# Optimization experiments

Measured on AMD Instinct MI355X. Metric: run time of the kernel, lower is better.

The kernel has to match this reference:

```python
import jax, jax.numpy as jnp
import numpy as np

B, Cin, C, H, W = 2, 64, 128, 64, 64
D_INNER, N_STATE, DT_RANK, K = 256, 16, 8, 4


def _silu(x):
    return x * jax.nn.sigmoid(x)


def _layernorm(x, g, b, eps=1e-5):
    mu = x.mean(-1, keepdims=True)
    var = ((x - mu) ** 2).mean(-1, keepdims=True)
    return (x - mu) * jax.lax.rsqrt(var + eps) * g + b


def setup_inputs():
    key = jax.random.key(0)
    ks = jax.random.split(key, 16)
    f32 = jnp.float32
    inp = {}
    inp["x"] = jax.random.normal(ks[0], (B, Cin, H, W), f32)
    inp["convin_w"] = jax.random.normal(ks[1], (C, Cin), f32) * 0.05
    inp["convin_b"] = jnp.zeros((C,), f32)
    inp["ln_g"] = jnp.ones((C,), f32)
    inp["ln_b"] = jnp.zeros((C,), f32)
    inp["in_proj_w"] = jax.random.normal(ks[2], (2 * D_INNER, C), f32) * 0.05
    inp["conv_w"] = jax.random.normal(ks[3], (D_INNER, 1, 3, 3), f32) * 0.1
    inp["conv_b"] = jnp.zeros((D_INNER,), f32)
    inp["x_proj_w"] = jax.random.normal(ks[4], (K, DT_RANK + 2 * N_STATE, D_INNER), f32) * 0.05
    inp["dt_w"] = jax.random.normal(ks[5], (K, D_INNER, DT_RANK), f32) * 0.1
    inp["dt_b"] = jax.random.uniform(ks[6], (K, D_INNER), f32, -4.0, -1.0)
    inp["A_logs"] = jnp.log(jnp.tile(jnp.arange(1, N_STATE + 1, dtype=f32), (K, D_INNER, 1)))
    inp["Ds"] = jnp.ones((K, D_INNER), f32)
    inp["outnorm_g"] = jnp.ones((D_INNER,), f32)
    inp["outnorm_b"] = jnp.zeros((D_INNER,), f32)
    inp["out_proj_w"] = jax.random.normal(ks[7], (C, D_INNER), f32) * 0.05
    inp["ca_fc1_w"] = jax.random.normal(ks[8], (C // 16, C), f32) * 0.1
    inp["ca_fc2_w"] = jax.random.normal(ks[9], (C, C // 16), f32) * 0.1
    inp["gn_g"] = jnp.ones((C,), f32)
    inp["gn_b"] = jnp.zeros((C,), f32)
    return inp


def _selective_scan(u, delta, A, Bm, Cm, Ds):
    # u, delta: (B,K,d,L); A: (K,d,N); Bm, Cm: (B,K,N,L); Ds: (K,d)
    def step(h, inp):
        u_t, dt, B_t, C_t = inp
        dA = jnp.exp(dt[..., None] * A)                      # (B,K,d,N)
        h = h * dA + dt[..., None] * B_t[:, :, None, :] * u_t[..., None]
        y = jnp.einsum('bkdn,bkn->bkd', h, C_t)
        return h, y
    step = jax.checkpoint(step)
    seq = (jnp.moveaxis(u, -1, 0), jnp.moveaxis(delta, -1, 0),
           jnp.moveaxis(Bm, -1, 0), jnp.moveaxis(Cm, -1, 0))
    h0 = jnp.zeros(u.shape[:3] + (A.shape[-1],), u.dtype)
    _, ys = jax.lax.scan(step, h0, seq)                      # (L,B,K,d)
    y = jnp.moveaxis(ys, 0, -1)                              # (B,K,d,L)
    return y + u * Ds[None, :, :, None]


def reference(x, convin_w, convin_b, ln_g, ln_b, in_proj_w, conv_w, conv_b,
              x_proj_w, dt_w, dt_b, A_logs, Ds, outnorm_g, outnorm_b,
              out_proj_w, ca_fc1_w, ca_fc2_w, gn_g, gn_b):
    L = H * W
    # 1x1 conv in
    x1 = jnp.einsum('bchw,oc->bohw', x, convin_w) + convin_b[None, :, None, None]
    m = x1.transpose(0, 2, 3, 1)                             # (B,H,W,C)
    # VSSBlock: LN -> SS2D -> residual
    m_ln = _layernorm(m, ln_g, ln_b)
    xz = m_ln @ in_proj_w.T                                  # (B,H,W,2*d_inner)
    xm, z = jnp.split(xz, 2, axis=-1)
    xm = xm.transpose(0, 3, 1, 2)                            # (B,d,H,W)
    xm = jax.lax.conv_general_dilated(xm, conv_w, (1, 1), [(1, 1), (1, 1)],
                                      feature_group_count=D_INNER)
    xm = _silu(xm + conv_b[None, :, None, None])
    x_flat = xm.reshape(B, D_INNER, L)
    x_tr = xm.transpose(0, 1, 3, 2).reshape(B, D_INNER, L)
    xs = jnp.stack([x_flat, x_tr, jnp.flip(x_flat, -1), jnp.flip(x_tr, -1)], axis=1)
    x_dbl = jnp.einsum('bkdl,kcd->bkcl', xs, x_proj_w)
    dts, Bs, Cs = jnp.split(x_dbl, [DT_RANK, DT_RANK + N_STATE], axis=2)
    delta = jax.nn.softplus(jnp.einsum('bkrl,kdr->bkdl', dts, dt_w) + dt_b[None, :, :, None])
    A = -jnp.exp(A_logs)                                     # (K,d,N)
    out_y = _selective_scan(xs, delta, A, Bs, Cs, Ds)        # (B,4,d,L)
    y0 = out_y[:, 0]
    y1 = out_y[:, 1].reshape(B, D_INNER, W, H).transpose(0, 1, 3, 2).reshape(B, D_INNER, L)
    y2 = jnp.flip(out_y[:, 2], -1)
    y3 = jnp.flip(out_y[:, 3], -1).reshape(B, D_INNER, W, H).transpose(0, 1, 3, 2).reshape(B, D_INNER, L)
    y = (y0 + y1 + y2 + y3).transpose(0, 2, 1).reshape(B, H, W, D_INNER)
    y = _layernorm(y, outnorm_g, outnorm_b)
    y = y * _silu(z)
    m_out = m + y @ out_proj_w.T                             # (B,H,W,C)
    mamba = m_out.transpose(0, 3, 1, 2)                      # (B,C,H,W)
    # CBAM-style channel attention
    def mlp(v):
        return jax.nn.relu(v @ ca_fc1_w.T) @ ca_fc2_w.T
    avg = mamba.mean((2, 3))
    mx = mamba.max((2, 3))
    att = jax.nn.sigmoid(mlp(avg) + mlp(mx))[:, :, None, None]
    ca = mamba * att
    # GroupNorm(2 groups) + SiLU + residual
    g = ca.reshape(B, 2, -1)
    mu = g.mean(-1, keepdims=True)
    var = ((g - mu) ** 2).mean(-1, keepdims=True)
    g = ((g - mu) * jax.lax.rsqrt(var + 1e-5)).reshape(B, C, H, W)
    g = g * gn_g[None, :, None, None] + gn_b[None, :, None, None]
    return _silu(g) + x1
```

## Files before the change

kernel.cpp:

```cpp
#include <hip/hip_runtime.h>
#include <math.h>


#define DEV __device__ __forceinline__

DEV float sigm_(float x){ return 1.f/(1.f+__expf(-x)); }
DEV float silu_(float x){ return x*sigm_(x); }
DEV float sp_(float x){ return (x>15.f)? x : __logf(1.f+__expf(x)); }

DEV int pos_dir(int k, int l){
  switch(k&3){
    case 0: return l;
    case 1: return ((l&63)<<6)|(l>>6);
    case 2: return 4095-l;
    default:{ int m=4095-l; return ((m&63)<<6)|(m>>6); }
  }
}

#define MM4x4(av,bv) do{ \
  acc[0][0]=fmaf(av.x,bv.x,acc[0][0]); acc[0][1]=fmaf(av.x,bv.y,acc[0][1]); \
  acc[0][2]=fmaf(av.x,bv.z,acc[0][2]); acc[0][3]=fmaf(av.x,bv.w,acc[0][3]); \
  acc[1][0]=fmaf(av.y,bv.x,acc[1][0]); acc[1][1]=fmaf(av.y,bv.y,acc[1][1]); \
  acc[1][2]=fmaf(av.y,bv.z,acc[1][2]); acc[1][3]=fmaf(av.y,bv.w,acc[1][3]); \
  acc[2][0]=fmaf(av.z,bv.x,acc[2][0]); acc[2][1]=fmaf(av.z,bv.y,acc[2][1]); \
  acc[2][2]=fmaf(av.z,bv.z,acc[2][2]); acc[2][3]=fmaf(av.z,bv.w,acc[2][3]); \
  acc[3][0]=fmaf(av.w,bv.x,acc[3][0]); acc[3][1]=fmaf(av.w,bv.y,acc[3][1]); \
  acc[3][2]=fmaf(av.w,bv.z,acc[3][2]); acc[3][3]=fmaf(av.w,bv.w,acc[3][3]); \
}while(0)

__global__ __launch_bounds__(256) void k_x1ln(const float* __restrict__ x,
    const float* __restrict__ W, const float* __restrict__ bias,
    const float* __restrict__ g, const float* __restrict__ be,
    float* __restrict__ x1, float* __restrict__ mln){
  const int b=blockIdx.y, p0=blockIdx.x*64;
  __shared__ float sw[64*132];
  __shared__ float sx[64*68];
  __shared__ float red[2][16][68];
  __shared__ float smu[64], srs[64];
  const int tid=threadIdx.x, tx=tid&15, ty=tid>>4;
  for (int i=tid;i<8192;i+=256){ int c=i&63,o=i>>6; sw[c*132+o]=W[o*64+c]; }
  for (int i=tid;i<4096;i+=256){ int c=i>>6,p=i&63; sx[c*68+p]=x[((size_t)(b*64+c))*4096+p0+p]; }
  __syncthreads();
  float acc[8][4]={};
  for (int c=0;c<64;++c){
    float4 a0=*(const float4*)&sw[c*132+ty*8];
    float4 a1=*(const float4*)&sw[c*132+ty*8+4];
    float4 bv=*(const float4*)&sx[c*68+tx*4];
    acc[0][0]=fmaf(a0.x,bv.x,acc[0][0]); acc[0][1]=fmaf(a0.x,bv.y,acc[0][1]); acc[0][2]=fmaf(a0.x,bv.z,acc[0][2]); acc[0][3]=fmaf(a0.x,bv.w,acc[0][3]);
    acc[1][0]=fmaf(a0.y,bv.x,acc[1][0]); acc[1][1]=fmaf(a0.y,bv.y,acc[1][1]); acc[1][2]=fmaf(a0.y,bv.z,acc[1][2]); acc[1][3]=fmaf(a0.y,bv.w,acc[1][3]);
    acc[2][0]=fmaf(a0.z,bv.x,acc[2][0]); acc[2][1]=fmaf(a0.z,bv.y,acc[2][1]); acc[2][2]=fmaf(a0.z,bv.z,acc[2][2]); acc[2][3]=fmaf(a0.z,bv.w,acc[2][3]);
    acc[3][0]=fmaf(a0.w,bv.x,acc[3][0]); acc[3][1]=fmaf(a0.w,bv.y,acc[3][1]); acc[3][2]=fmaf(a0.w,bv.z,acc[3][2]); acc[3][3]=fmaf(a0.w,bv.w,acc[3][3]);
    acc[4][0]=fmaf(a1.x,bv.x,acc[4][0]); acc[4][1]=fmaf(a1.x,bv.y,acc[4][1]); acc[4][2]=fmaf(a1.x,bv.z,acc[4][2]); acc[4][3]=fmaf(a1.x,bv.w,acc[4][3]);
    acc[5][0]=fmaf(a1.y,bv.x,acc[5][0]); acc[5][1]=fmaf(a1.y,bv.y,acc[5][1]); acc[5][2]=fmaf(a1.y,bv.z,acc[5][2]); acc[5][3]=fmaf(a1.y,bv.w,acc[5][3]);
    acc[6][0]=fmaf(a1.z,bv.x,acc[6][0]); acc[6][1]=fmaf(a1.z,bv.y,acc[6][1]); acc[6][2]=fmaf(a1.z,bv.z,acc[6][2]); acc[6][3]=fmaf(a1.z,bv.w,acc[6][3]);
    acc[7][0]=fmaf(a1.w,bv.x,acc[7][0]); acc[7][1]=fmaf(a1.w,bv.y,acc[7][1]); acc[7][2]=fmaf(a1.w,bv.z,acc[7][2]); acc[7][3]=fmaf(a1.w,bv.w,acc[7][3]);
  }
  float xr[8][4];
  #pragma unroll
  for (int i=0;i<8;++i){
    float bs=bias[ty*8+i];
    #pragma unroll
    for (int j=0;j<4;++j) xr[i][j]=acc[i][j]+bs;
  }
  {
    float s[4]={},s2[4]={};
    #pragma unroll
    for (int i=0;i<8;++i)
      #pragma unroll
      for (int j=0;j<4;++j){ s[j]+=xr[i][j]; s2[j]=fmaf(xr[i][j],xr[i][j],s2[j]); }
    #pragma unroll
    for (int j=0;j<4;++j){ red[0][ty][tx*4+j]=s[j]; red[1][ty][tx*4+j]=s2[j]; }
  }
  __syncthreads();
  if (tid<64){
    float S=0.f,S2=0.f;
    #pragma unroll
    for (int t=0;t<16;++t){ S+=red[0][t][tid]; S2+=red[1][t][tid]; }
    float mu=S*(1.f/128.f), var=S2*(1.f/128.f)-mu*mu;
    smu[tid]=mu; srs[tid]=rsqrtf(var+1e-5f);
  }
  __syncthreads();
  float* lnt=sw;
  #pragma unroll
  for (int i=0;i<8;++i){
    int o=ty*8+i;
    float gv=g[o], bev=be[o];
    #pragma unroll
    for (int j=0;j<4;++j){
      int p=tx*4+j;
      lnt[o*66+p]=(xr[i][j]-smu[p])*srs[p]*gv+bev;
    }
    *(float4*)&x1[((size_t)(b*128+o))*4096+p0+tx*4]=make_float4(xr[i][0],xr[i][1],xr[i][2],xr[i][3]);
  }
  __syncthreads();
  for (int i=tid;i<8192;i+=256){ int p=i>>7,o=i&127; mln[((size_t)(b*4096+p0+p))*128+o]=lnt[o*66+p]; }
}

__global__ __launch_bounds__(256) void k_inproj(const float* __restrict__ mln,
    const float* __restrict__ W, float* __restrict__ xmpre_t, float* __restrict__ z){
  const int m0=blockIdx.y*64, n0=blockIdx.x*64;
  __shared__ float As[16][68], Bs[16][68];
  const int tid=threadIdx.x, tx=tid&15, ty=tid>>4;
  float acc[4][4]={};
  for (int k0=0;k0<128;k0+=16){
    for (int i=tid;i<64*16;i+=256){ int m=i>>4,k=i&15; As[k][m]=mln[(size_t)(m0+m)*128+(k0+k)]; }
    for (int i=tid;i<64*16;i+=256){ int n=i>>4,k=i&15; Bs[k][n]=W[(size_t)(n0+n)*128+(k0+k)]; }
    __syncthreads();
    #pragma unroll
    for (int k=0;k<16;++k){
      float4 av=*(const float4*)&As[k][ty*4];
      float4 bv=*(const float4*)&Bs[k][tx*4];
      MM4x4(av,bv);
    }
    __syncthreads();
  }
  const int col=n0+tx*4;
  #pragma unroll
  for (int i=0;i<4;++i){
    int row=m0+ty*4+i;
    float4 v=make_float4(acc[i][0],acc[i][1],acc[i][2],acc[i][3]);
    if (col<256) *(float4*)&xmpre_t[(size_t)row*256+col]=v;
    else         *(float4*)&z[(size_t)row*256+(col-256)]=v;
  }
}

__global__ __launch_bounds__(256) void k_dwconv(const float* __restrict__ xmpre_t,
    const float* __restrict__ cw, const float* __restrict__ cb, float* __restrict__ xflat_t){
  __shared__ float sw[2304];
  __shared__ float sb[256];
  const int tid=threadIdx.x;
  for (int i=tid;i<2304;i+=256) sw[i]=cw[i];
  sb[tid]=cb[tid];
  __syncthreads();
  const int bp0=blockIdx.x*16;
  const int b=bp0>>12, p0=bp0&4095;
  const int dq=tid&63, pg=tid>>6;
  const int d0=dq*4;
  float wr[9][4];
  #pragma unroll
  for (int t=0;t<9;++t)
    #pragma unroll
    for (int c=0;c<4;++c) wr[t][c]=sw[(d0+c)*9+t];
  const float4 bias=make_float4(sb[d0],sb[d0+1],sb[d0+2],sb[d0+3]);
  #pragma unroll
  for (int j=0;j<4;++j){
    const int p=p0+pg*4+j;
    const int h=p>>6, w=p&63;
    float4 acc=bias;
    #pragma unroll
    for (int dh=-1;dh<=1;++dh){
      int hh=h+dh; if ((unsigned)hh>=64u) continue;
      #pragma unroll
      for (int dw=-1;dw<=1;++dw){
        int ww=w+dw; if ((unsigned)ww>=64u) continue;
        const int t=(dh+1)*3+(dw+1);
        float4 iv=*(const float4*)&xmpre_t[((size_t)((b<<12)+hh*64+ww))*256+d0];
        acc.x=fmaf(iv.x,wr[t][0],acc.x); acc.y=fmaf(iv.y,wr[t][1],acc.y);
        acc.z=fmaf(iv.z,wr[t][2],acc.z); acc.w=fmaf(iv.w,wr[t][3],acc.w);
      }
    }
    acc.x=silu_(acc.x); acc.y=silu_(acc.y); acc.z=silu_(acc.z); acc.w=silu_(acc.w);
    *(float4*)&xflat_t[((size_t)((b<<12)+p))*256+d0]=acc;
  }
}

__global__ __launch_bounds__(256) void k_proj(const float* __restrict__ xflat_t,
    const float* __restrict__ xpw, float* __restrict__ pdt, float* __restrict__ pbc){
  const int b=blockIdx.z, n0=blockIdx.y*32, m0=blockIdx.x*64;
  __shared__ float As[16][68], Bs[16][36];
  const int tid=threadIdx.x, tx=tid&15, ty=tid>>4;
  float acc[4][2]={};
  for (int k0=0;k0<256;k0+=16){
    for (int i=tid;i<64*16;i+=256){ int m=i>>4,kk=i&15; As[kk][m]=xflat_t[((size_t)((b<<12)+m0+m))*256+k0+kk]; }
    for (int i=tid;i<32*16;i+=256){ int n=i>>4,kk=i&15; Bs[kk][n]=xpw[(size_t)(n0+n)*256+k0+kk]; }
    __syncthreads();
    #pragma unroll
    for (int kk=0;kk<16;++kk){
      float4 av=*(const float4*)&As[kk][ty*4];
      float2 bv=*(const float2*)&Bs[kk][tx*2];
      acc[0][0]=fmaf(av.x,bv.x,acc[0][0]); acc[0][1]=fmaf(av.x,bv.y,acc[0][1]);
      acc[1][0]=fmaf(av.y,bv.x,acc[1][0]); acc[1][1]=fmaf(av.y,bv.y,acc[1][1]);
      acc[2][0]=fmaf(av.z,bv.x,acc[2][0]); acc[2][1]=fmaf(av.z,bv.y,acc[2][1]);
      acc[3][0]=fmaf(av.w,bv.x,acc[3][0]); acc[3][1]=fmaf(av.w,bv.y,acc[3][1]);
    }
    __syncthreads();
  }
  #pragma unroll
  for (int i=0;i<4;++i){
    int l=m0+ty*4+i;
    #pragma unroll
    for (int j=0;j<2;++j){
      int r=n0+tx*2+j, kd=r/40, c=r%40, bk=b*4+kd;
      float v=acc[i][j];
      if (c<8) pdt[((size_t)bk*4096+l)*8+c]=v;
      else     pbc[((size_t)bk*4096+l)*32+(c-8)]=v;
    }
  }
}

__global__ __launch_bounds__(256) void k_scanA(const float* __restrict__ pdt,
    const float* __restrict__ pbc, const float* __restrict__ xflat_t,
    const float* __restrict__ dtw, const float* __restrict__ dtb,
    const float* __restrict__ A_logs, const float* __restrict__ Ds,
    float* __restrict__ Pc, float* __restrict__ He, float* __restrict__ y4){
  const int bx=blockIdx.x;
  const int ch=bx&127, k=(bx>>7)&3, b=bx>>9, bk=b*4+k;
  const int d=threadIdx.x;
  __shared__ float sbc[1024];
  __shared__ float sdt[256];
  for (int i=d;i<1024;i+=256) sbc[i]=pbc[((size_t)bk*4096+(ch<<5))*32+i];
  sdt[d]=pdt[((size_t)bk*4096+(ch<<5))*8+d];
  const float* ap=&A_logs[((k<<8)+d)<<4];
  const float ac0=-__expf(ap[0]);
  bool pw=true;
  #pragma unroll
  for (int n=1;n<16;++n){ float an_=-__expf(ap[n]); pw=pw&&(fabsf(an_-(float)(n+1)*ac0)<=1e-4f*fabsf(an_)); }
  float w8[8];
  {
    float4 w0=*(const float4*)&dtw[(size_t)k*2048+d*8];
    float4 w1=*(const float4*)&dtw[(size_t)k*2048+d*8+4];
    w8[0]=w0.x;w8[1]=w0.y;w8[2]=w0.z;w8[3]=w0.w;w8[4]=w1.x;w8[5]=w1.y;w8[6]=w1.z;w8[7]=w1.w;
  }
  const float dtbd=dtb[(k<<8)+d];
  const float dsv=Ds[(k<<8)+d];
  __syncthreads();
  float h[16]; float sdv=0.f;
  #pragma unroll
  for (int n=0;n<16;++n) h[n]=0.f;
  const float* up=xflat_t+((size_t)b<<12)*256+d;
  if (pw){
    for (int s=0;s<32;++s){
      const int l=(ch<<5)+s;
      float t=dtbd;
      #pragma unroll
      for (int r=0;r<8;++r) t=fmaf(sdt[s*8+r],w8[r],t);
      const float dv=sp_(t);
      const float u=up[(size_t)pos_dir(k,l)*256];
      const float dvu=dv*u;
      sdv+=dv;
      const float q=__expf(dv*ac0);
      float an=q, yl=0.f;
      #pragma unroll
      for (int n4=0;n4<4;++n4){
        float4 bb=*(const float4*)&sbc[s*32+n4*4];
        float4 cc=*(const float4*)&sbc[s*32+16+n4*4];
        h[n4*4+0]=fmaf(h[n4*4+0],an,dvu*bb.x); yl=fmaf(h[n4*4+0],cc.x,yl); an*=q;
        h[n4*4+1]=fmaf(h[n4*4+1],an,dvu*bb.y); yl=fmaf(h[n4*4+1],cc.y,yl); an*=q;
        h[n4*4+2]=fmaf(h[n4*4+2],an,dvu*bb.z); yl=fmaf(h[n4*4+2],cc.z,yl); an*=q;
        h[n4*4+3]=fmaf(h[n4*4+3],an,dvu*bb.w); yl=fmaf(h[n4*4+3],cc.w,yl); an*=q;
      }
      y4[((size_t)((b<<12)+pos_dir(k,l))*4+k)*256+d]=yl+u*dsv;
    }
  } else {
    float acoef[16];
    #pragma unroll
    for (int n=0;n<16;++n) acoef[n]=-__expf(ap[n]);
    for (int s=0;s<32;++s){
      const int l=(ch<<5)+s;
      float t=dtbd;
      #pragma unroll
      for (int r=0;r<8;++r) t=fmaf(sdt[s*8+r],w8[r],t);
      const float dv=sp_(t);
      const float u=up[(size_t)pos_dir(k,l)*256];
      const float dvu=dv*u;
      sdv+=dv;
      float yl=0.f;
      #pragma unroll
      for (int n=0;n<16;++n){
        float a=__expf(dv*acoef[n]);
        h[n]=fmaf(h[n],a,dvu*sbc[s*32+n]);
        yl=fmaf(h[n],sbc[s*32+16+n],yl);
      }
      y4[((size_t)((b<<12)+pos_dir(k,l))*4+k)*256+d]=yl+u*dsv;
    }
  }
  const size_t obase=(size_t)ch*32768 + ((size_t)bk*256+d)*16;
  if (pw){
    const float qe=__expf(ac0*sdv);
    float an=qe, pcv[16];
    #pragma unroll
    for (int n=0;n<16;++n){ pcv[n]=an; an*=qe; }
    #pragma unroll
    for (int n4=0;n4<4;++n4) *(float4*)&Pc[obase+n4*4]=make_float4(pcv[n4*4],pcv[n4*4+1],pcv[n4*4+2],pcv[n4*4+3]);
  } else {
    #pragma unroll
    for (int n=0;n<16;++n) Pc[obase+n]=__expf(-__expf(ap[n])*sdv);
  }
  #pragma unroll
  for (int n4=0;n4<4;++n4) *(float4*)&He[obase+n4*4]=make_float4(h[n4*4],h[n4*4+1],h[n4*4+2],h[n4*4+3]);
}

__global__ __launch_bounds__(256) void k_scanB(const float* Pc, const float* He, float* Hin){
  const int g2=threadIdx.x&63, tc=threadIdx.x>>6;
  const int gid=blockIdx.x*64+g2;
  float p[32], e[32];
  #pragma unroll
  for (int i=0;i<32;++i){
    size_t idx=(size_t)(tc*32+i)*32768+gid;
    p[i]=Pc[idx]; e[i]=He[idx];
  }
  float P=1.f, E=0.f;
  #pragma unroll
  for (int i=0;i<32;++i){ E=fmaf(E,p[i],e[i]); P*=p[i]; }
  __shared__ float sP[4][64], sE[4][64];
  sP[tc][g2]=P; sE[tc][g2]=E;
  __syncthreads();
  float Hp=0.f;
  for (int t=0;t<tc;++t) Hp=fmaf(Hp,sP[t][g2],sE[t][g2]);
  #pragma unroll
  for (int i=0;i<32;++i){
    Hin[(size_t)(tc*32+i)*32768+gid]=Hp;
    Hp=fmaf(Hp,p[i],e[i]);
  }
}

__global__ __launch_bounds__(256) void k_scanC2(const float* __restrict__ pdt,
    const float* __restrict__ pbc, const float* __restrict__ dtw,
    const float* __restrict__ dtb, const float* __restrict__ A_logs,
    const float* __restrict__ Hin, float* __restrict__ y4){
  const int bx=blockIdx.x;
  const int ch=bx&127, k=(bx>>7)&3, b=bx>>9, bk=b*4+k;
  if (ch==0) return;
  const int d=threadIdx.x;
  __shared__ float sC[512];
  __shared__ float sdt[256];
  for (int i=d;i<512;i+=256){ int s=i>>4,n=i&15; sC[i]=pbc[((size_t)bk*4096+(ch<<5)+s)*32+16+n]; }
  sdt[d]=pdt[((size_t)bk*4096+(ch<<5))*8+d];
  const float* ap=&A_logs[((k<<8)+d)<<4];
  const float ac0=-__expf(ap[0]);
  bool pw=true;
  #pragma unroll
  for (int n=1;n<16;++n){ float an_=-__expf(ap[n]); pw=pw&&(fabsf(an_-(float)(n+1)*ac0)<=1e-4f*fabsf(an_)); }
  float w8[8];
  {
    float4 w0=*(const float4*)&dtw[(size_t)k*2048+d*8];
    float4 w1=*(const float4*)&dtw[(size_t)k*2048+d*8+4];
    w8[0]=w0.x;w8[1]=w0.y;w8[2]=w0.z;w8[3]=w0.w;w8[4]=w1.x;w8[5]=w1.y;w8[6]=w1.z;w8[7]=w1.w;
  }
  const float dtbd=dtb[(k<<8)+d];
  __syncthreads();
  const size_t ibase=(size_t)ch*32768 + ((size_t)bk*256+d)*16;
  float h[16];
  #pragma unroll
  for (int n4=0;n4<4;++n4){
    float4 hv=*(const float4*)&Hin[ibase+n4*4];
    h[n4*4]=hv.x; h[n4*4+1]=hv.y; h[n4*4+2]=hv.z; h[n4*4+3]=hv.w;
  }
  if (pw){
    float cumd=0.f;
    for (int s=0;s<32;++s){
      float t=dtbd;
      #pragma unroll
      for (int r=0;r<8;++r) t=fmaf(sdt[s*8+r],w8[r],t);
      cumd+=sp_(t);
      const float q=__expf(ac0*cumd);
      float an=q, corr=0.f;
      #pragma unroll
      for (int n4=0;n4<4;++n4){
        float4 cc=*(const float4*)&sC[s*16+n4*4];
        corr=fmaf(h[n4*4+0]*an,cc.x,corr); an*=q;
        corr=fmaf(h[n4*4+1]*an,cc.y,corr); an*=q;
        corr=fmaf(h[n4*4+2]*an,cc.z,corr); an*=q;
        corr=fmaf(h[n4*4+3]*an,cc.w,corr); an*=q;
      }
      const int l=(ch<<5)+s;
      y4[((size_t)((b<<12)+pos_dir(k,l))*4+k)*256+d]+=corr;
    }
  } else {
    float acoef[16];
    #pragma unroll
    for (int n=0;n<16;++n) acoef[n]=-__expf(ap[n]);
    float cumd=0.f;
    for (int s=0;s<32;++s){
      float t=dtbd;
      #pragma unroll
      for (int r=0;r<8;++r) t=fmaf(sdt[s*8+r],w8[r],t);
      cumd+=sp_(t);
      float corr=0.f;
      #pragma unroll
      for (int n=0;n<16;++n) corr=fmaf(h[n]*__expf(acoef[n]*cumd),sC[s*16+n],corr);
      const int l=(ch<<5)+s;
      y4[((size_t)((b<<12)+pos_dir(k,l))*4+k)*256+d]+=corr;
    }
  }
}

__global__ __launch_bounds__(256) void k_outnorm(const float* __restrict__ y4,
    const float* __restrict__ g, const float* __restrict__ be,
    const float* __restrict__ z, float* __restrict__ yg){
  const int bp=blockIdx.x, d=threadIdx.x;
  const float* base=y4+(size_t)bp*1024;
  float v=base[d]+base[256+d]+base[512+d]+base[768+d];
  float s=v, s2=v*v;
  #pragma unroll
  for (int m=1;m<64;m<<=1){ s+=__shfl_xor(s,m); s2+=__shfl_xor(s2,m); }
  __shared__ float rs[4], rs2[4];
  if ((d&63)==0){ rs[d>>6]=s; rs2[d>>6]=s2; }
  __syncthreads();
  float S=rs[0]+rs[1]+rs[2]+rs[3], S2=rs2[0]+rs2[1]+rs2[2]+rs2[3];
  float mu=S*(1.f/256.f), var=S2*(1.f/256.f)-mu*mu, rstd=rsqrtf(var+1e-5f);
  float ln=(v-mu)*rstd*g[d]+be[d];
  float zv=z[(size_t)bp*256+d];
  yg[(size_t)bp*256+d]=ln*silu_(zv);
}

__global__ __launch_bounds__(256) void k_outproj(const float* __restrict__ yg,
    const float* __restrict__ W, const float* __restrict__ x1, float* __restrict__ mamba){
  const int b=blockIdx.z, m0=blockIdx.y*64, n0=blockIdx.x*64;
  __shared__ float As[16][68], Bs[16][68];
  const int tid=threadIdx.x, tx=tid&15, ty=tid>>4;
  float acc[4][4]={};
  const float* Yb=yg+(size_t)(b<<12)*256;
  for (int k0=0;k0<256;k0+=16){
    for (int i=tid;i<64*16;i+=256){ int m=i>>4,k=i&15; As[k][m]=W[(size_t)(m0+m)*256+(k0+k)]; }
    for (int i=tid;i<64*16;i+=256){ int n=i>>4,k=i&15; Bs[k][n]=Yb[(size_t)(n0+n)*256+(k0+k)]; }
    __syncthreads();
    #pragma unroll
    for (int k=0;k<16;++k){
      float4 av=*(const float4*)&As[k][ty*4];
      float4 bv=*(const float4*)&Bs[k][tx*4];
      MM4x4(av,bv);
    }
    __syncthreads();
  }
  #pragma unroll
  for (int i=0;i<4;++i){
    int c=m0+ty*4+i;
    size_t base=(size_t)((b<<7)+c)*4096 + n0+tx*4;
    float4 xv=*(const float4*)&x1[base];
    float4 v=make_float4(acc[i][0]+xv.x,acc[i][1]+xv.y,acc[i][2]+xv.z,acc[i][3]+xv.w);
    *(float4*)&mamba[base]=v;
  }
}

__global__ __launch_bounds__(256) void k_stats(const float* __restrict__ mamba, float* __restrict__ stats){
  const int bc=blockIdx.x, tid=threadIdx.x;
  const float* row=mamba+(size_t)bc*4096;
  float s=0.f,s2=0.f,mx=-3.402823466e38f;
  for (int i=tid;i<4096;i+=256){ float v=row[i]; s+=v; s2=fmaf(v,v,s2); mx=fmaxf(mx,v); }
  #pragma unroll
  for (int m=1;m<64;m<<=1){
    s+=__shfl_xor(s,m); s2+=__shfl_xor(s2,m); mx=fmaxf(mx,__shfl_xor(mx,m));
  }
  __shared__ float r0[4],r1[4],r2[4];
  if ((tid&63)==0){ int wv=tid>>6; r0[wv]=s; r1[wv]=s2; r2[wv]=mx; }
  __syncthreads();
  if (tid==0){
    stats[bc*3+0]=r0[0]+r0[1]+r0[2]+r0[3];
    stats[bc*3+1]=r1[0]+r1[1]+r1[2]+r1[3];
    stats[bc*3+2]=fmaxf(fmaxf(r2[0],r2[1]),fmaxf(r2[2],r2[3]));
  }
}

__global__ __launch_bounds__(256) void k_att(const float* __restrict__ stats,
    const float* __restrict__ fc1, const float* __restrict__ fc2,
    float* __restrict__ att, float* __restrict__ gstat){
  __shared__ float avg[2][128], mxs[2][128], S1[2][128], S2[2][128], hsum[2][8], attv[2][128];
  const int tid=threadIdx.x, b=tid>>7, c=tid&127;
  float s1=stats[tid*3], s2=stats[tid*3+1], m=stats[tid*3+2];
  avg[b][c]=s1*(1.f/4096.f); mxs[b][c]=m; S1[b][c]=s1; S2[b][c]=s2;
  __syncthreads();
  if (tid<16){
    int bb=tid>>3, i=tid&7;
    float ha=0.f,hm=0.f;
    for (int cc=0;cc<128;++cc){ float w=fc1[i*128+cc]; ha=fmaf(w,avg[bb][cc],ha); hm=fmaf(w,mxs[bb][cc],hm); }
    hsum[bb][i]=fmaxf(ha,0.f)+fmaxf(hm,0.f);
  }
  __syncthreads();
  float sacc=0.f;
  #pragma unroll
  for (int i=0;i<8;++i) sacc=fmaf(fc2[c*8+i],hsum[b][i],sacc);
  float a=sigm_(sacc);
  attv[b][c]=a; att[tid]=a;
  __syncthreads();
  if (tid<4){
    int bb=tid>>1, gp=tid&1;
    float sum1=0.f,sum2=0.f;
    for (int cc=0;cc<64;++cc){
      int c2=gp*64+cc; float av=attv[bb][c2];
      sum1=fmaf(av,S1[bb][c2],sum1);
      sum2=fmaf(av*av,S2[bb][c2],sum2);
    }
    const float inv=1.f/(64.f*4096.f);
    float mu=sum1*inv, ex2=sum2*inv, var=ex2-mu*mu;
    gstat[tid*2]=mu; gstat[tid*2+1]=rsqrtf(var+1e-5f);
  }
}

__global__ __launch_bounds__(256) void k_final(const float* __restrict__ mamba,
    const float* __restrict__ x1, const float* __restrict__ att,
    const float* __restrict__ gstat, const float* __restrict__ gg,
    const float* __restrict__ gb, float* __restrict__ out){
  const int idx=blockIdx.x*256+threadIdx.x;
  const int c=(idx>>12)&127, b=idx>>19;
  const int grp=(b<<1)+(c>>6);
  float v=mamba[idx]*att[(b<<7)+c];
  float vn=(v-gstat[grp*2])*gstat[grp*2+1]*gg[c]+gb[c];
  out[idx]=silu_(vn)+x1[idx];
}

extern "C" void kernel_launch(void* const* d_in, const int* in_sizes, int n_in,
                              void* d_out, int out_size, void* d_ws, size_t ws_size,
                              hipStream_t stream){
  (void)in_sizes; (void)n_in; (void)out_size; (void)ws_size;
  const float* x        =(const float*)d_in[0];
  const float* convin_w =(const float*)d_in[1];
  const float* convin_b =(const float*)d_in[2];
  const float* ln_g     =(const float*)d_in[3];
  const float* ln_b     =(const float*)d_in[4];
  const float* in_proj_w=(const float*)d_in[5];
  const float* conv_w   =(const float*)d_in[6];
  const float* conv_b   =(const float*)d_in[7];
  const float* x_proj_w =(const float*)d_in[8];
  const float* dt_w     =(const float*)d_in[9];
  const float* dt_b     =(const float*)d_in[10];
  const float* A_logs   =(const float*)d_in[11];
  const float* Ds       =(const float*)d_in[12];
  const float* outnorm_g=(const float*)d_in[13];
  const float* outnorm_b=(const float*)d_in[14];
  const float* out_proj_w=(const float*)d_in[15];
  const float* ca_fc1_w =(const float*)d_in[16];
  const float* ca_fc2_w =(const float*)d_in[17];
  const float* gn_g     =(const float*)d_in[18];
  const float* gn_b     =(const float*)d_in[19];

  float* ws=(float*)d_ws;
  float* x1     =ws+0;
  float* z      =ws+1048576;
  float* xmpre_t=ws+3145728;
  float* mln    =ws+5242880;
  float* xflat_t=ws+6291456;
  float* pdt    =ws+8388608;
  float* pbc    =ws+8912896;
  float* Pc     =ws+10485760;
  float* He     =ws+14680064;
  float* y4     =ws+18874368;
  float* yg     =ws+3145728;
  float* mamba  =ws+5242880;
  float* stats  =ws+27262976;
  float* att    =stats+768;
  float* gstat  =att+256;

  const dim3 blk(256);
  k_x1ln   <<<dim3(64,2),   blk,0,stream>>>(x, convin_w, convin_b, ln_g, ln_b, x1, mln);
  k_inproj <<<dim3(8,128),  blk,0,stream>>>(mln, in_proj_w, xmpre_t, z);
  k_dwconv <<<dim3(512),    blk,0,stream>>>(xmpre_t, conv_w, conv_b, xflat_t);
  k_proj   <<<dim3(64,5,2), blk,0,stream>>>(xflat_t, x_proj_w, pdt, pbc);
  k_scanA  <<<dim3(1024),   blk,0,stream>>>(pdt, pbc, xflat_t, dt_w, dt_b, A_logs, Ds, Pc, He, y4);
  k_scanB  <<<dim3(512),    blk,0,stream>>>(Pc, He, Pc );
  k_scanC2 <<<dim3(1024),   blk,0,stream>>>(pdt, pbc, dt_w, dt_b, A_logs, Pc , y4);
  k_outnorm<<<dim3(8192),   blk,0,stream>>>(y4, outnorm_g, outnorm_b, z, yg);
  k_outproj<<<dim3(64,2,2), blk,0,stream>>>(yg, out_proj_w, x1, mamba);
  k_stats  <<<dim3(256),    blk,0,stream>>>(mamba, stats);
  k_att    <<<dim3(1),      blk,0,stream>>>(stats, ca_fc1_w, ca_fc2_w, att, gstat);
  k_final  <<<dim3(4096),   blk,0,stream>>>(mamba, x1, att, gstat, gn_g, gn_b, (float*)d_out);
}
```

Before: 301.7 us.

## Use bf16 MFMA for projections and atomically accumulate scan outputs

Replaces the three FP32 shared-memory SIMT GEMMs (in_proj, x_proj, out_proj) with bf16 MFMA 16x16x32 kernels that load fragments straight from global memory. The intermediate activations (LN output, conv output, gated output) are stored as bf16, halving their traffic. The scan kernels now atomically add into a single summed y buffer instead of writing four per-direction copies, which drops the 4-way read in outnorm at the cost of atomic contention and an extra memset. The changes trade accuracy (bf16 operands), and per-lane scalar epilogue stores are less coalesced.

```diff
diff --git a/kernel.cpp b/kernel.cpp
--- a/kernel.cpp
+++ b/kernel.cpp
@@ -3,10 +3,20 @@
 
 
 #define DEV __device__ __forceinline__
+
+typedef __attribute__((ext_vector_type(8))) short bf16x8;
+typedef __attribute__((ext_vector_type(4))) float f32x4;
 
 DEV float sigm_(float x){ return 1.f/(1.f+__expf(-x)); }
 DEV float silu_(float x){ return x*sigm_(x); }
 DEV float sp_(float x){ return (x>15.f)? x : __logf(1.f+__expf(x)); }
+
+DEV unsigned short f2bf(float f){
+  union{float f; unsigned u;} v; v.f=f;
+  unsigned r=v.u + 0x7FFFu + ((v.u>>16)&1u);
+  return (unsigned short)(r>>16);
+}
+DEV float bf2f(unsigned short h){ union{unsigned u; float f;} v; v.u=((unsigned)h)<<16; return v.f; }
 
 DEV int pos_dir(int k, int l){
   switch(k&3){
@@ -17,21 +27,18 @@
   }
 }
 
-#define MM4x4(av,bv) do{ \
-  acc[0][0]=fmaf(av.x,bv.x,acc[0][0]); acc[0][1]=fmaf(av.x,bv.y,acc[0][1]); \
-  acc[0][2]=fmaf(av.x,bv.z,acc[0][2]); acc[0][3]=fmaf(av.x,bv.w,acc[0][3]); \
-  acc[1][0]=fmaf(av.y,bv.x,acc[1][0]); acc[1][1]=fmaf(av.y,bv.y,acc[1][1]); \
-  acc[1][2]=fmaf(av.y,bv.z,acc[1][2]); acc[1][3]=fmaf(av.y,bv.w,acc[1][3]); \
-  acc[2][0]=fmaf(av.z,bv.x,acc[2][0]); acc[2][1]=fmaf(av.z,bv.y,acc[2][1]); \
-  acc[2][2]=fmaf(av.z,bv.z,acc[2][2]); acc[2][3]=fmaf(av.z,bv.w,acc[2][3]); \
-  acc[3][0]=fmaf(av.w,bv.x,acc[3][0]); acc[3][1]=fmaf(av.w,bv.y,acc[3][1]); \
-  acc[3][2]=fmaf(av.w,bv.z,acc[3][2]); acc[3][3]=fmaf(av.w,bv.w,acc[3][3]); \
-}while(0)
+DEV bf16x8 cvt_frag(const float* p){
+  float4 q0=*(const float4*)p, q1=*(const float4*)(p+4);
+  bf16x8 t;
+  t[0]=(short)f2bf(q0.x); t[1]=(short)f2bf(q0.y); t[2]=(short)f2bf(q0.z); t[3]=(short)f2bf(q0.w);
+  t[4]=(short)f2bf(q1.x); t[5]=(short)f2bf(q1.y); t[6]=(short)f2bf(q1.z); t[7]=(short)f2bf(q1.w);
+  return t;
+}
 
 __global__ __launch_bounds__(256) void k_x1ln(const float* __restrict__ x,
     const float* __restrict__ W, const float* __restrict__ bias,
     const float* __restrict__ g, const float* __restrict__ be,
-    float* __restrict__ x1, float* __restrict__ mln){
+    float* __restrict__ x1, unsigned short* __restrict__ mlnb){
   const int b=blockIdx.y, p0=blockIdx.x*64;
   __shared__ float sw[64*132];
   __shared__ float sx[64*68];
@@ -93,39 +100,50 @@
     *(float4*)&x1[((size_t)(b*128+o))*4096+p0+tx*4]=make_float4(xr[i][0],xr[i][1],xr[i][2],xr[i][3]);
   }
   __syncthreads();
-  for (int i=tid;i<8192;i+=256){ int p=i>>7,o=i&127; mln[((size_t)(b*4096+p0+p))*128+o]=lnt[o*66+p]; }
-}
-
-__global__ __launch_bounds__(256) void k_inproj(const float* __restrict__ mln,
+  for (int i=tid;i<8192;i+=256){ int p=i>>7,o=i&127; mlnb[((size_t)(b*4096+p0+p))*128+o]=f2bf(lnt[o*66+p]); }
+}
+
+__global__ __launch_bounds__(256) void k_inproj(const unsigned short* __restrict__ mlnb,
     const float* __restrict__ W, float* __restrict__ xmpre_t, float* __restrict__ z){
-  const int m0=blockIdx.y*64, n0=blockIdx.x*64;
-  __shared__ float As[16][68], Bs[16][68];
-  const int tid=threadIdx.x, tx=tid&15, ty=tid>>4;
-  float acc[4][4]={};
-  for (int k0=0;k0<128;k0+=16){
-    for (int i=tid;i<64*16;i+=256){ int m=i>>4,k=i&15; As[k][m]=mln[(size_t)(m0+m)*128+(k0+k)]; }
-    for (int i=tid;i<64*16;i+=256){ int n=i>>4,k=i&15; Bs[k][n]=W[(size_t)(n0+n)*128+(k0+k)]; }
-    __syncthreads();
-    #pragma unroll
-    for (int k=0;k<16;++k){
-      float4 av=*(const float4*)&As[k][ty*4];
-      float4 bv=*(const float4*)&Bs[k][tx*4];
-      MM4x4(av,bv);
-    }
-    __syncthreads();
-  }
-  const int col=n0+tx*4;
-  #pragma unroll
-  for (int i=0;i<4;++i){
-    int row=m0+ty*4+i;
-    float4 v=make_float4(acc[i][0],acc[i][1],acc[i][2],acc[i][3]);
-    if (col<256) *(float4*)&xmpre_t[(size_t)row*256+col]=v;
-    else         *(float4*)&z[(size_t)row*256+(col-256)]=v;
-  }
+  const int wave=threadIdx.x>>6, lane=threadIdx.x&63;
+  const int quad=lane>>4, l16=lane&15;
+  const int m0=blockIdx.y*128+(wave>>1)*64;
+  const int n0=blockIdx.x*64+(wave&1)*32;
+  f32x4 acc[4][2];
+  #pragma unroll
+  for (int i=0;i<4;++i)
+    #pragma unroll
+    for (int j=0;j<2;++j) acc[i][j]=(f32x4){0.f,0.f,0.f,0.f};
+  for (int k0=0;k0<128;k0+=32){
+    bf16x8 a[4], b[2];
+    #pragma unroll
+    for (int mi=0;mi<4;++mi)
+      a[mi]=*(const bf16x8*)&mlnb[(size_t)(m0+mi*16+l16)*128 + k0 + quad*8];
+    #pragma unroll
+    for (int ni=0;ni<2;++ni)
+      b[ni]=cvt_frag(&W[(size_t)(n0+ni*16+l16)*128 + k0 + quad*8]);
+    #pragma unroll
+    for (int mi=0;mi<4;++mi)
+      #pragma unroll
+      for (int ni=0;ni<2;++ni)
+        acc[mi][ni]=__builtin_amdgcn_mfma_f32_16x16x32_bf16(a[mi],b[ni],acc[mi][ni],0,0,0);
+  }
+  #pragma unroll
+  for (int mi=0;mi<4;++mi)
+    #pragma unroll
+    for (int ni=0;ni<2;++ni)
+      #pragma unroll
+      for (int r=0;r<4;++r){
+        const int row=m0+mi*16+quad*4+r;
+        const int col=n0+ni*16+l16;
+        float v=acc[mi][ni][r];
+        if (col<256) xmpre_t[(size_t)row*256+col]=v;
+        else         z[(size_t)row*256+(col-256)]=v;
+      }
 }
 
 __global__ __launch_bounds__(256) void k_dwconv(const float* __restrict__ xmpre_t,
-    const float* __restrict__ cw, const float* __restrict__ cb, float* __restrict__ xflat_t){
+    const float* __restrict__ cw, const float* __restrict__ cb, unsigned short* __restrict__ xflatb){
   __shared__ float sw[2304];
   __shared__ float sb[256];
   const int tid=threadIdx.x;
@@ -159,50 +177,58 @@
         acc.z=fmaf(iv.z,wr[t][2],acc.z); acc.w=fmaf(iv.w,wr[t][3],acc.w);
       }
     }
-    acc.x=silu_(acc.x); acc.y=silu_(acc.y); acc.z=silu_(acc.z); acc.w=silu_(acc.w);
-    *(float4*)&xflat_t[((size_t)((b<<12)+p))*256+d0]=acc;
-  }
-}
-
-__global__ __launch_bounds__(256) void k_proj(const float* __restrict__ xflat_t,
+    ushort4 o;
+    o.x=f2bf(silu_(acc.x)); o.y=f2bf(silu_(acc.y)); o.z=f2bf(silu_(acc.z)); o.w=f2bf(silu_(acc.w));
+    *(ushort4*)&xflatb[((size_t)((b<<12)+p))*256+d0]=o;
+  }
+}
+
+__global__ __launch_bounds__(256) void k_proj(const unsigned short* __restrict__ xflatb,
     const float* __restrict__ xpw, float* __restrict__ pdt, float* __restrict__ pbc){
-  const int b=blockIdx.z, n0=blockIdx.y*32, m0=blockIdx.x*64;
-  __shared__ float As[16][68], Bs[16][36];
-  const int tid=threadIdx.x, tx=tid&15, ty=tid>>4;
-  float acc[4][2]={};
-  for (int k0=0;k0<256;k0+=16){
-    for (int i=tid;i<64*16;i+=256){ int m=i>>4,kk=i&15; As[kk][m]=xflat_t[((size_t)((b<<12)+m0+m))*256+k0+kk]; }
-    for (int i=tid;i<32*16;i+=256){ int n=i>>4,kk=i&15; Bs[kk][n]=xpw[(size_t)(n0+n)*256+k0+kk]; }
-    __syncthreads();
-    #pragma unroll
-    for (int kk=0;kk<16;++kk){
-      float4 av=*(const float4*)&As[kk][ty*4];
-      float2 bv=*(const float2*)&Bs[kk][tx*2];
-      acc[0][0]=fmaf(av.x,bv.x,acc[0][0]); acc[0][1]=fmaf(av.x,bv.y,acc[0][1]);
-      acc[1][0]=fmaf(av.y,bv.x,acc[1][0]); acc[1][1]=fmaf(av.y,bv.y,acc[1][1]);
-      acc[2][0]=fmaf(av.z,bv.x,acc[2][0]); acc[2][1]=fmaf(av.z,bv.y,acc[2][1]);
-      acc[3][0]=fmaf(av.w,bv.x,acc[3][0]); acc[3][1]=fmaf(av.w,bv.y,acc[3][1]);
-    }
-    __syncthreads();
-  }
-  #pragma unroll
-  for (int i=0;i<4;++i){
-    int l=m0+ty*4+i;
-    #pragma unroll
-    for (int j=0;j<2;++j){
-      int r=n0+tx*2+j, kd=r/40, c=r%40, bk=b*4+kd;
-      float v=acc[i][j];
-      if (c<8) pdt[((size_t)bk*4096+l)*8+c]=v;
-      else     pbc[((size_t)bk*4096+l)*32+(c-8)]=v;
-    }
-  }
+  const int wave=threadIdx.x>>6, lane=threadIdx.x&63;
+  const int quad=lane>>4, l16=lane&15;
+  const int m0=(wave&1)*80;
+  const int n0=blockIdx.x*64+(wave>>1)*32;
+  f32x4 acc[5][2];
+  #pragma unroll
+  for (int i=0;i<5;++i)
+    #pragma unroll
+    for (int j=0;j<2;++j) acc[i][j]=(f32x4){0.f,0.f,0.f,0.f};
+  for (int k0=0;k0<256;k0+=32){
+    bf16x8 a[5], b[2];
+    #pragma unroll
+    for (int mi=0;mi<5;++mi)
+      a[mi]=cvt_frag(&xpw[(size_t)(m0+mi*16+l16)*256 + k0 + quad*8]);
+    #pragma unroll
+    for (int ni=0;ni<2;++ni)
+      b[ni]=*(const bf16x8*)&xflatb[(size_t)(n0+ni*16+l16)*256 + k0 + quad*8];
+    #pragma unroll
+    for (int mi=0;mi<5;++mi)
+      #pragma unroll
+      for (int ni=0;ni<2;++ni)
+        acc[mi][ni]=__builtin_amdgcn_mfma_f32_16x16x32_bf16(a[mi],b[ni],acc[mi][ni],0,0,0);
+  }
+  #pragma unroll
+  for (int mi=0;mi<5;++mi)
+    #pragma unroll
+    for (int ni=0;ni<2;++ni)
+      #pragma unroll
+      for (int r=0;r<4;++r){
+        const int rr=m0+mi*16+quad*4+r;
+        const int col=n0+ni*16+l16;
+        const int b_=col>>12, pos=col&4095;
+        const int kd=rr/40, c=rr%40, bk=b_*4+kd;
+        float v=acc[mi][ni][r];
+        if (c<8) pdt[((size_t)bk*4096+pos)*8+c]=v;
+        else     pbc[((size_t)bk*4096+pos)*32+(c-8)]=v;
+      }
 }
 
 __global__ __launch_bounds__(256) void k_scanA(const float* __restrict__ pdt,
-    const float* __restrict__ pbc, const float* __restrict__ xflat_t,
+    const float* __restrict__ pbc, const unsigned short* __restrict__ xflatb,
     const float* __restrict__ dtw, const float* __restrict__ dtb,
     const float* __restrict__ A_logs, const float* __restrict__ Ds,
-    float* __restrict__ Pc, float* __restrict__ He, float* __restrict__ y4){
+    float* __restrict__ Pc, float* __restrict__ He, float* __restrict__ ysum){
   const int bx=blockIdx.x;
   const int ch=bx&127, k=(bx>>7)&3, b=bx>>9, bk=b*4+k;
   const int d=threadIdx.x;
@@ -227,7 +253,7 @@
   float h[16]; float sdv=0.f;
   #pragma unroll
   for (int n=0;n<16;++n) h[n]=0.f;
-  const float* up=xflat_t+((size_t)b<<12)*256+d;
+  const unsigned short* up=xflatb+((size_t)b<<12)*256+d;
   if (pw){
     for (int s=0;s<32;++s){
       const int l=(ch<<5)+s;
@@ -235,7 +261,8 @@
       #pragma unroll
       for (int r=0;r<8;++r) t=fmaf(sdt[s*8+r],w8[r],t);
       const float dv=sp_(t);
-      const float u=up[(size_t)pos_dir(k,l)*256];
+      const int pos=pos_dir(k,l);
+      const float u=bf2f(up[(size_t)pos*256]);
       const float dvu=dv*u;
       sdv+=dv;
       const float q=__expf(dv*ac0);
@@ -249,7 +276,7 @@
         h[n4*4+2]=fmaf(h[n4*4+2],an,dvu*bb.z); yl=fmaf(h[n4*4+2],cc.z,yl); an*=q;
         h[n4*4+3]=fmaf(h[n4*4+3],an,dvu*bb.w); yl=fmaf(h[n4*4+3],cc.w,yl); an*=q;
       }
-      y4[((size_t)((b<<12)+pos_dir(k,l))*4+k)*256+d]=yl+u*dsv;
+      atomicAdd(&ysum[((size_t)((b<<12)+pos))*256+d], yl+u*dsv);
     }
   } else {
     float acoef[16];
@@ -261,7 +288,8 @@
       #pragma unroll
       for (int r=0;r<8;++r) t=fmaf(sdt[s*8+r],w8[r],t);
       const float dv=sp_(t);
-      const float u=up[(size_t)pos_dir(k,l)*256];
+      const int pos=pos_dir(k,l);
+      const float u=bf2f(up[(size_t)pos*256]);
       const float dvu=dv*u;
       sdv+=dv;
       float yl=0.f;
@@ -271,7 +299,7 @@
         h[n]=fmaf(h[n],a,dvu*sbc[s*32+n]);
         yl=fmaf(h[n],sbc[s*32+16+n],yl);
       }
-      y4[((size_t)((b<<12)+pos_dir(k,l))*4+k)*256+d]=yl+u*dsv;
+      atomicAdd(&ysum[((size_t)((b<<12)+pos))*256+d], yl+u*dsv);
     }
   }
   const size_t obase=(size_t)ch*32768 + ((size_t)bk*256+d)*16;
@@ -317,7 +345,7 @@
 __global__ __launch_bounds__(256) void k_scanC2(const float* __restrict__ pdt,
     const float* __restrict__ pbc, const float* __restrict__ dtw,
     const float* __restrict__ dtb, const float* __restrict__ A_logs,
-    const float* __restrict__ Hin, float* __restrict__ y4){
+    const float* __restrict__ Hin, float* __restrict__ ysum){
   const int bx=blockIdx.x;
   const int ch=bx&127, k=(bx>>7)&3, b=bx>>9, bk=b*4+k;
   if (ch==0) return;
@@ -364,7 +392,7 @@
         corr=fmaf(h[n4*4+3]*an,cc.w,corr); an*=q;
       }
       const int l=(ch<<5)+s;
-      y4[((size_t)((b<<12)+pos_dir(k,l))*4+k)*256+d]+=corr;
+      atomicAdd(&ysum[((size_t)((b<<12)+pos_dir(k,l)))*256+d], corr);
     }
   } else {
     float acoef[16];
@@ -380,17 +408,16 @@
       #pragma unroll
       for (int n=0;n<16;++n) corr=fmaf(h[n]*__expf(acoef[n]*cumd),sC[s*16+n],corr);
       const int l=(ch<<5)+s;
-      y4[((size_t)((b<<12)+pos_dir(k,l))*4+k)*256+d]+=corr;
-    }
-  }
-}
-
-__global__ __launch_bounds__(256) void k_outnorm(const float* __restrict__ y4,
+      atomicAdd(&ysum[((size_t)((b<<12)+pos_dir(k,l)))*256+d], corr);
+    }
+  }
+}
+
+__global__ __launch_bounds__(256) void k_outnorm(const float* __restrict__ ysum,
     const float* __restrict__ g, const float* __restrict__ be,
-    const float* __restrict__ z, float* __restrict__ yg){
+    const float* __restrict__ z, unsigned short* __restrict__ ygb){
   const int bp=blockIdx.x, d=threadIdx.x;
-  const float* base=y4+(size_t)bp*1024;
-  float v=base[d]+base[256+d]+base[512+d]+base[768+d];
+  float v=ysum[(size_t)bp*256+d];
   float s=v, s2=v*v;
   #pragma unroll
   for (int m=1;m<64;m<<=1){ s+=__shfl_xor(s,m); s2+=__shfl_xor(s2,m); }
@@ -401,36 +428,46 @@
   float mu=S*(1.f/256.f), var=S2*(1.f/256.f)-mu*mu, rstd=rsqrtf(var+1e-5f);
   float ln=(v-mu)*rstd*g[d]+be[d];
   float zv=z[(size_t)bp*256+d];
-  yg[(size_t)bp*256+d]=ln*silu_(zv);
-}
-
-__global__ __launch_bounds__(256) void k_outproj(const float* __restrict__ yg,
+  ygb[(size_t)bp*256+d]=f2bf(ln*silu_(zv));
+}
+
+__global__ __launch_bounds__(256) void k_outproj(const unsigned short* __restrict__ ygb,
     const float* __restrict__ W, const float* __restrict__ x1, float* __restrict__ mamba){
-  const int b=blockIdx.z, m0=blockIdx.y*64, n0=blockIdx.x*64;
-  __shared__ float As[16][68], Bs[16][68];
-  const int tid=threadIdx.x, tx=tid&15, ty=tid>>4;
-  float acc[4][4]={};
-  const float* Yb=yg+(size_t)(b<<12)*256;
-  for (int k0=0;k0<256;k0+=16){
-    for (int i=tid;i<64*16;i+=256){ int m=i>>4,k=i&15; As[k][m]=W[(size_t)(m0+m)*256+(k0+k)]; }
-    for (int i=tid;i<64*16;i+=256){ int n=i>>4,k=i&15; Bs[k][n]=Yb[(size_t)(n0+n)*256+(k0+k)]; }
-    __syncthreads();
-    #pragma unroll
-    for (int k=0;k<16;++k){
-      float4 av=*(const float4*)&As[k][ty*4];
-      float4 bv=*(const float4*)&Bs[k][tx*4];
-      MM4x4(av,bv);
-    }
-    __syncthreads();
-  }
-  #pragma unroll
-  for (int i=0;i<4;++i){
-    int c=m0+ty*4+i;
-    size_t base=(size_t)((b<<7)+c)*4096 + n0+tx*4;
-    float4 xv=*(const float4*)&x1[base];
-    float4 v=make_float4(acc[i][0]+xv.x,acc[i][1]+xv.y,acc[i][2]+xv.z,acc[i][3]+xv.w);
-    *(float4*)&mamba[base]=v;
-  }
+  const int wave=threadIdx.x>>6, lane=threadIdx.x&63;
+  const int quad=lane>>4, l16=lane&15;
+  const int m0=(wave>>1)*64;
+  const int n0=blockIdx.x*64+(wave&1)*32;
+  f32x4 acc[4][2];
+  #pragma unroll
+  for (int i=0;i<4;++i)
+    #pragma unroll
+    for (int j=0;j<2;++j) acc[i][j]=(f32x4){0.f,0.f,0.f,0.f};
+  for (int k0=0;k0<256;k0+=32){
+    bf16x8 a[4], b[2];
+    #pragma unroll
+    for (int mi=0;mi<4;++mi)
+      a[mi]=cvt_frag(&W[(size_t)(m0+mi*16+l16)*256 + k0 + quad*8]);
+    #pragma unroll
+    for (int ni=0;ni<2;++ni)
+      b[ni]=*(const bf16x8*)&ygb[(size_t)(n0+ni*16+l16)*256 + k0 + quad*8];
+    #pragma unroll
+    for (int mi=0;mi<4;++mi)
+      #pragma unroll
+      for (int ni=0;ni<2;++ni)
+        acc[mi][ni]=__builtin_amdgcn_mfma_f32_16x16x32_bf16(a[mi],b[ni],acc[mi][ni],0,0,0);
+  }
+  #pragma unroll
+  for (int mi=0;mi<4;++mi)
+    #pragma unroll
+    for (int ni=0;ni<2;++ni)
+      #pragma unroll
+      for (int r=0;r<4;++r){
+        const int c=m0+mi*16+quad*4+r;
+        const int col=n0+ni*16+l16;
+        const int b_=col>>12, pos=col&4095;
+        const size_t addr=((size_t)((b_<<7)+c))*4096+pos;
+        mamba[addr]=acc[mi][ni][r]+x1[addr];
+      }
 }
 
 __global__ __launch_bounds__(256) void k_stats(const float* __restrict__ mamba, float* __restrict__ stats){
@@ -525,32 +562,33 @@
   const float* gn_b     =(const float*)d_in[19];
 
   float* ws=(float*)d_ws;
-  float* x1     =ws+0;
-  float* z      =ws+1048576;
-  float* xmpre_t=ws+3145728;
-  float* mln    =ws+5242880;
-  float* xflat_t=ws+6291456;
-  float* pdt    =ws+8388608;
-  float* pbc    =ws+8912896;
-  float* Pc     =ws+10485760;
-  float* He     =ws+14680064;
-  float* y4     =ws+18874368;
-  float* yg     =ws+3145728;
-  float* mamba  =ws+5242880;
-  float* stats  =ws+27262976;
-  float* att    =stats+768;
-  float* gstat  =att+256;
+  float*          x1     =ws+0;
+  float*          z      =ws+1048576;
+  float*          xmpre_t=ws+3145728;
+  unsigned short* mlnb   =(unsigned short*)(ws+5242880);
+  unsigned short* xflatb =(unsigned short*)(ws+6291456);
+  float*          pdt    =ws+8388608;
+  float*          pbc    =ws+8912896;
+  float*          Pc     =ws+10485760;
+  float*          He     =ws+14680064;
+  float*          ysum   =ws+18874368;
+  unsigned short* ygb    =(unsigned short*)(ws+3145728);
+  float*          mamba  =ws+5242880;
+  float*          stats  =ws+27262976;
+  float*          att    =stats+768;
+  float*          gstat  =att+256;
 
   const dim3 blk(256);
-  k_x1ln   <<<dim3(64,2),   blk,0,stream>>>(x, convin_w, convin_b, ln_g, ln_b, x1, mln);
-  k_inproj <<<dim3(8,128),  blk,0,stream>>>(mln, in_proj_w, xmpre_t, z);
-  k_dwconv <<<dim3(512),    blk,0,stream>>>(xmpre_t, conv_w, conv_b, xflat_t);
-  k_proj   <<<dim3(64,5,2), blk,0,stream>>>(xflat_t, x_proj_w, pdt, pbc);
-  k_scanA  <<<dim3(1024),   blk,0,stream>>>(pdt, pbc, xflat_t, dt_w, dt_b, A_logs, Ds, Pc, He, y4);
+  hipMemsetAsync(ysum, 0, 2097152*sizeof(float), stream);
+  k_x1ln   <<<dim3(64,2),   blk,0,stream>>>(x, convin_w, convin_b, ln_g, ln_b, x1, mlnb);
+  k_inproj <<<dim3(8,64),   blk,0,stream>>>(mlnb, in_proj_w, xmpre_t, z);
+  k_dwconv <<<dim3(512),    blk,0,stream>>>(xmpre_t, conv_w, conv_b, xflatb);
+  k_proj   <<<dim3(128),    blk,0,stream>>>(xflatb, x_proj_w, pdt, pbc);
+  k_scanA  <<<dim3(1024),   blk,0,stream>>>(pdt, pbc, xflatb, dt_w, dt_b, A_logs, Ds, Pc, He, ysum);
   k_scanB  <<<dim3(512),    blk,0,stream>>>(Pc, He, Pc );
-  k_scanC2 <<<dim3(1024),   blk,0,stream>>>(pdt, pbc, dt_w, dt_b, A_logs, Pc , y4);
-  k_outnorm<<<dim3(8192),   blk,0,stream>>>(y4, outnorm_g, outnorm_b, z, yg);
-  k_outproj<<<dim3(64,2,2), blk,0,stream>>>(yg, out_proj_w, x1, mamba);
+  k_scanC2 <<<dim3(1024),   blk,0,stream>>>(pdt, pbc, dt_w, dt_b, A_logs, Pc , ysum);
+  k_outnorm<<<dim3(8192),   blk,0,stream>>>(ysum, outnorm_g, outnorm_b, z, ygb);
+  k_outproj<<<dim3(128),    blk,0,stream>>>(ygb, out_proj_w, x1, mamba);
   k_stats  <<<dim3(256),    blk,0,stream>>>(mamba, stats);
   k_att    <<<dim3(1),      blk,0,stream>>>(stats, ca_fc1_w, ca_fc2_w, att, gstat);
   k_final  <<<dim3(4096),   blk,0,stream>>>(mamba, x1, att, gstat, gn_g, gn_b, (float*)d_out);
```

Result: faster. 269.6 us (-10.7%).
